# Performance work log

Measured on AMD Instinct MI355X. Metric: run time of the kernel, lower is better.

The kernel has to match this reference:

```python
import jax, jax.numpy as jnp
import numpy as np
import math

HEADS = 10
EPS = 1e-5
SHARED_SCORE_SHIFT = 0.6931471805599453  # log(2)


def expand_first(feat):
    # feat: [B, ...]; batch split into two halves, first element of each half is the style reference
    b = feat.shape[0]
    style = jnp.stack([feat[0], feat[b // 2]])[:, None]  # [2, 1, ...]
    style = jnp.broadcast_to(style, (2, b // 2) + feat.shape[1:])
    return style.reshape(feat.shape)


def adain(feat):
    # feat: [B, H, S, D]; normalize over seq dim (-2), re-style with reference stats
    mean = feat.mean(axis=-2, keepdims=True)
    std = jnp.sqrt(jnp.var(feat, axis=-2, keepdims=True, ddof=1) + EPS)
    style_mean = expand_first(mean)
    style_std = expand_first(std)
    return (feat - mean) / std * style_std + style_mean


def concat_first(feat, axis=2):
    # scale == 1.0 path of concat_first
    return jnp.concatenate([feat, expand_first(feat)], axis=axis)


def setup_inputs() -> dict:
    key = jax.random.key(0)
    ks = jax.random.split(key, 9)
    B, S, C = 4, 1024, 640
    sc = 1.0 / math.sqrt(C)
    return {
        "hidden_states": jax.random.normal(ks[0], (B, S, C), jnp.float32),
        "Wq": jax.random.normal(ks[1], (C, C), jnp.float32) * sc,
        "bq": jax.random.normal(ks[2], (C,), jnp.float32) * 0.01,
        "Wk": jax.random.normal(ks[3], (C, C), jnp.float32) * sc,
        "bk": jax.random.normal(ks[4], (C,), jnp.float32) * 0.01,
        "Wv": jax.random.normal(ks[5], (C, C), jnp.float32) * sc,
        "bv": jax.random.normal(ks[6], (C,), jnp.float32) * 0.01,
        "Wo": jax.random.normal(ks[7], (C, C), jnp.float32) * sc,
        "bo": jax.random.normal(ks[8], (C,), jnp.float32) * 0.01,
    }


def reference(hidden_states, Wq, bq, Wk, bk, Wv, bv, Wo, bo):
    B, S, C = hidden_states.shape
    H = HEADS
    D = C // H
    scale = 1.0 / math.sqrt(D)  # attn.scale

    def split_heads(x):  # [B, S, C] -> [B, H, S, D]
        return x.reshape(B, S, H, D).transpose(0, 2, 1, 3)

    q = split_heads(hidden_states @ Wq.T + bq)
    k = split_heads(hidden_states @ Wk.T + bk)
    v = split_heads(hidden_states @ Wv.T + bv)

    # adain_queries / adain_keys enabled, adain_values disabled
    q = adain(q)
    k = adain(k)

    # shared attention: concatenate reference K/V along seq dim
    k = concat_first(k, axis=2)  # [B, H, 2S, D]
    v = concat_first(v, axis=2)

    logits = jnp.einsum('bhqd,bhkd->bhqk', q, k) * scale
    # additive shift on the shared (appended) keys
    kv_len = k.shape[2]
    shift = jnp.where(jnp.arange(kv_len) >= S, SHARED_SCORE_SHIFT, 0.0).astype(logits.dtype)
    logits = logits + shift
    probs = jax.nn.softmax(logits, axis=-1)
    out = jnp.einsum('bhqk,bhkd->bhqd', probs, v)  # [B, H, S, D]

    out = out.transpose(0, 2, 1, 3).reshape(B, S, C)
    return out @ Wo.T + bo
```

## Files before the change

### kernel.cpp

```cpp
#include <hip/hip_runtime.h>
#include <hip/hip_bf16.h>
#include <math.h>

typedef unsigned short u16;
typedef unsigned int u32;
typedef __attribute__((ext_vector_type(8))) short short8;
typedef __attribute__((ext_vector_type(4))) float float4_;

#define S_LEN 1024
#define C_DIM 640
#define HEADS 10
#define HDIM 64
#define M_TOT 4096
#define WSZ (C_DIM * C_DIM)
#define TX ((size_t)M_TOT * C_DIM)
#define SHIFT_C 0.6931471805599453f
#define LDG 44
#define LDA 76
#define PS  (2 * S_LEN * C_DIM)
#define LS  (2 * HEADS * S_LEN)

static __device__ __forceinline__ float bf2f(u16 u) {
    unsigned int x = ((unsigned int)u) << 16;
    float f; __builtin_memcpy(&f, &x, 4); return f;
}
static __device__ __forceinline__ u16 f2bf(float f) {
    unsigned int x; __builtin_memcpy(&x, &f, 4);
    x = x + 0x7fffu + ((x >> 16) & 1u);
    return (u16)(x >> 16);
}

static __device__ int detect_bf16(const void* X) {
    const u32* p = (const u32*)X;
    int sane = 0;
    for (int i = 0; i < 64; i++) {
        u32 w = p[i];
        int ea = (int)((w >> 7)  & 0xFF);
        int eb = (int)((w >> 23) & 0xFF);
        sane += (ea >= 100 && ea <= 150);
        sane += (eb >= 100 && eb <= 150);
    }
    return sane >= 110;
}

__global__ __launch_bounds__(256) void convert_inputs(
    const void* X, const void* W0, const void* W1, const void* W2, const void* W3,
    const void* B0, const void* B1, const void* B2, const void* B3,
    u16* __restrict__ Xb, u16* __restrict__ Wb, float* __restrict__ Bf,
    int* __restrict__ flag)
{
    __shared__ int is_bf;
    if (threadIdx.x == 0) {
        int f = detect_bf16(X);
        is_bf = f;
        if (blockIdx.x == 0) *flag = f;
    }
    __syncthreads();
    const int f = is_bf;

    const size_t WREG = TX + 4 * (size_t)WSZ;
    const size_t TOT  = WREG + 4 * C_DIM;
    size_t idx8 = ((size_t)blockIdx.x * 256 + threadIdx.x) * 8;
    if (idx8 >= TOT) return;

    const void* src; size_t off; int kind;
    u16* dst16 = nullptr; float* dstf = nullptr;
    if (idx8 < TX) {
        src = X; off = idx8; dst16 = Xb + off; kind = 0;
    } else if (idx8 < WREG) {
        size_t r = idx8 - TX; int w = (int)(r / WSZ); off = r % WSZ;
        src = (w == 0) ? W0 : ((w == 1) ? W1 : ((w == 2) ? W2 : W3));
        dst16 = Wb + (size_t)w * WSZ + off; kind = 0;
    } else {
        size_t r = idx8 - WREG; int w = (int)(r / C_DIM); off = r % C_DIM;
        src = (w == 0) ? B0 : ((w == 1) ? B1 : ((w == 2) ? B2 : B3));
        dstf = Bf + (size_t)w * C_DIM + off; kind = 1;
    }

    if (!f) {
        float4 a = *(const float4*)((const float*)src + off);
        float4 b = *(const float4*)((const float*)src + off + 4);
        if (kind == 0) {
            union { u16 s[8]; uint4 u; } pk;
            pk.s[0] = f2bf(a.x); pk.s[1] = f2bf(a.y); pk.s[2] = f2bf(a.z); pk.s[3] = f2bf(a.w);
            pk.s[4] = f2bf(b.x); pk.s[5] = f2bf(b.y); pk.s[6] = f2bf(b.z); pk.s[7] = f2bf(b.w);
            *(uint4*)dst16 = pk.u;
        } else {
            *(float4*)dstf = a; *(float4*)(dstf + 4) = b;
        }
    } else {
        union { uint4 u; u16 s[8]; } pk;
        pk.u = *(const uint4*)((const u16*)src + off);
        if (kind == 0) {
            *(uint4*)dst16 = pk.u;
        } else {
            #pragma unroll
            for (int j = 0; j < 8; j++) dstf[j] = bf2f(pk.s[j]);
        }
    }
}

__global__ __launch_bounds__(256, 3) void gemm_bt(
    const u16* __restrict__ A, const u16* __restrict__ Wbase,
    const float* __restrict__ Bf,
    u16* Oq, u16* Ok, u16* Vt, float* Of, const int* __restrict__ flag,
    int final_mode)
{
    const int z = final_mode ? 3 : blockIdx.z;
    const u16* W    = Wbase + (size_t)z * WSZ;
    const float* bias = Bf + (size_t)z * C_DIM;

    __shared__ u16 Al[2][128 * LDG];
    __shared__ u16 Wl[2][128 * LDG];

    const int tid  = threadIdx.x;
    const int wave = tid >> 6;
    const int lane = tid & 63;
    const int l16  = lane & 15;
    const int quad = lane >> 4;
    const int m0 = blockIdx.x * 128;
    const int n0 = blockIdx.y * 128;
    const int wm = (wave & 1) * 64;
    const int wn = (wave >> 1) * 64;

    const int srow = tid >> 2;
    const int scol = (tid & 3) * 8;

    float4_ acc[4][4] = {};
    uint4 va[2], vw[2];

    #pragma unroll
    for (int i = 0; i < 2; i++) {
        int row = srow + i * 64;
        va[i] = *(const uint4*)(A + (size_t)(m0 + row) * C_DIM + scol);
        vw[i] = *(const uint4*)(W + (size_t)(n0 + row) * C_DIM + scol);
    }
    #pragma unroll
    for (int i = 0; i < 2; i++) {
        int row = srow + i * 64;
        *(uint4*)(&Al[0][row * LDG + scol]) = va[i];
        *(uint4*)(&Wl[0][row * LDG + scol]) = vw[i];
    }

    const int NIT = C_DIM / 32;
    for (int kt = 0; kt < NIT; kt++) {
        const int buf = kt & 1;
        __syncthreads();

        if (kt + 1 < NIT) {
            int k0 = (kt + 1) * 32;
            #pragma unroll
            for (int i = 0; i < 2; i++) {
                int row = srow + i * 64;
                va[i] = *(const uint4*)(A + (size_t)(m0 + row) * C_DIM + k0 + scol);
                vw[i] = *(const uint4*)(W + (size_t)(n0 + row) * C_DIM + k0 + scol);
            }
        }

        short8 af[4], bfr[4];
        #pragma unroll
        for (int t = 0; t < 4; t++) {
            af[t]  = *(const short8*)(&Al[buf][(wm + t * 16 + l16) * LDG + quad * 8]);
            bfr[t] = *(const short8*)(&Wl[buf][(wn + t * 16 + l16) * LDG + quad * 8]);
        }
        #pragma unroll
        for (int mt = 0; mt < 4; mt++)
            #pragma unroll
            for (int nt = 0; nt < 4; nt++)
                acc[mt][nt] = __builtin_amdgcn_mfma_f32_16x16x32_bf16(
                    af[mt], bfr[nt], acc[mt][nt], 0, 0, 0);

        if (kt + 1 < NIT) {
            #pragma unroll
            for (int i = 0; i < 2; i++) {
                int row = srow + i * 64;
                *(uint4*)(&Al[buf ^ 1][row * LDG + scol]) = va[i];
                *(uint4*)(&Wl[buf ^ 1][row * LDG + scol]) = vw[i];
            }
        }
    }

    const bool wf32 = final_mode && (*flag == 0);
    #pragma unroll
    for (int mt = 0; mt < 4; mt++) {
        #pragma unroll
        for (int nt = 0; nt < 4; nt++) {
            int col = n0 + wn + nt * 16 + l16;
            float bv = bias[col];
            if (!final_mode && z == 2) {
                int row0 = m0 + wm + mt * 16 + quad * 4;
                int bb = row0 >> 10, s = row0 & 1023;
                ushort4 pk;
                pk.x = f2bf(acc[mt][nt][0] + bv);
                pk.y = f2bf(acc[mt][nt][1] + bv);
                pk.z = f2bf(acc[mt][nt][2] + bv);
                pk.w = f2bf(acc[mt][nt][3] + bv);
                *(ushort4*)(Vt + ((size_t)(bb * C_DIM + col)) * S_LEN + s) = pk;
            } else {
                #pragma unroll
                for (int r = 0; r < 4; r++) {
                    int row = m0 + wm + mt * 16 + quad * 4 + r;
                    float val = acc[mt][nt][r] + bv;
                    size_t idx = (size_t)row * C_DIM + col;
                    if (final_mode) {
                        if (wf32) Of[idx] = val;
                        else      Oq[idx] = f2bf(val);
                    } else {
                        u16* Out = (z == 0) ? Oq : Ok;
                        Out[idx] = f2bf(val);
                    }
                }
            }
        }
    }
}

__global__ __launch_bounds__(1024) void adain_stats(
    const u16* __restrict__ Qp, const u16* __restrict__ Kp,
    float* __restrict__ meanArr, float* __restrict__ stdArr)
{
    const int bid = blockIdx.x;
    const int t = bid / 40;
    const int rem = bid % 40;
    const int b = rem / 10;
    const int h = rem % 10;
    const u16* X = t ? Kp : Qp;

    const int tid = threadIdx.x;
    const int do8 = tid & 7;
    const int sg  = tid >> 3;

    const u16* base = X + (size_t)(b * S_LEN) * C_DIM + h * HDIM + do8 * 8;
    float s8[8] = {}, q8[8] = {};
    #pragma unroll
    for (int i = 0; i < 8; i++) {
        int s = sg + i * 128;
        union { uint4 u; u16 e[8]; } v;
        v.u = *(const uint4*)(base + (size_t)s * C_DIM);
        #pragma unroll
        for (int j = 0; j < 8; j++) {
            float f = bf2f(v.e[j]);
            s8[j] += f; q8[j] += f * f;
        }
    }
    #pragma unroll
    for (int off = 8; off < 64; off <<= 1)
        #pragma unroll
        for (int j = 0; j < 8; j++) {
            s8[j] += __shfl_xor(s8[j], off, 64);
            q8[j] += __shfl_xor(q8[j], off, 64);
        }
    __shared__ float ls[16][64], lq[16][64];
    const int wv = tid >> 6, ln = tid & 63;
    if (ln < 8) {
        #pragma unroll
        for (int j = 0; j < 8; j++) { ls[wv][ln * 8 + j] = s8[j]; lq[wv][ln * 8 + j] = q8[j]; }
    }
    __syncthreads();
    if (tid < 64) {
        float Sv = 0.f, Qv = 0.f;
        #pragma unroll
        for (int g = 0; g < 16; g++) { Sv += ls[g][tid]; Qv += lq[g][tid]; }
        float mean = Sv * (1.f / 1024.f);
        float var  = (Qv - Sv * Sv * (1.f / 1024.f)) * (1.f / 1023.f);
        int idx = ((t * 4 + b) * HEADS + h) * HDIM + tid;
        meanArr[idx] = mean;
        stdArr[idx]  = sqrtf(fmaxf(var, 0.f) + 1e-5f);
    }
}

__global__ __launch_bounds__(256) void adain_apply(
    u16* __restrict__ Qp, u16* __restrict__ Kp,
    const float* __restrict__ meanArr, const float* __restrict__ stdArr)
{
    const size_t idx8 = ((size_t)blockIdx.x * 256 + threadIdx.x) * 8;
    const int t  = (int)(idx8 / (2 * S_LEN * C_DIM));
    const int r  = (int)(idx8 % (2 * S_LEN * C_DIM));
    const int bi = r / (S_LEN * C_DIM);
    const int r2 = r % (S_LEN * C_DIM);
    const int s  = r2 / C_DIM;
    const int c  = r2 % C_DIM;
    const int b  = bi * 2 + 1;
    const int h  = c >> 6, d = c & 63;

    u16* X = t ? Kp : Qp;
    const int si   = ((t * 4 + b) * HEADS + h) * HDIM + d;
    const int sref = ((t * 4 + (b - 1)) * HEADS + h) * HDIM + d;

    float4 stT0 = *(const float4*)(stdArr + si);
    float4 stT1 = *(const float4*)(stdArr + si + 4);
    float4 stR0 = *(const float4*)(stdArr + sref);
    float4 stR1 = *(const float4*)(stdArr + sref + 4);
    float4 mnT0 = *(const float4*)(meanArr + si);
    float4 mnT1 = *(const float4*)(meanArr + si + 4);
    float4 mnR0 = *(const float4*)(meanArr + sref);
    float4 mnR1 = *(const float4*)(meanArr + sref + 4);
    float sc[8], of[8];
    sc[0]=stR0.x/stT0.x; sc[1]=stR0.y/stT0.y; sc[2]=stR0.z/stT0.z; sc[3]=stR0.w/stT0.w;
    sc[4]=stR1.x/stT1.x; sc[5]=stR1.y/stT1.y; sc[6]=stR1.z/stT1.z; sc[7]=stR1.w/stT1.w;
    of[0]=mnR0.x-mnT0.x*sc[0]; of[1]=mnR0.y-mnT0.y*sc[1];
    of[2]=mnR0.z-mnT0.z*sc[2]; of[3]=mnR0.w-mnT0.w*sc[3];
    of[4]=mnR1.x-mnT1.x*sc[4]; of[5]=mnR1.y-mnT1.y*sc[5];
    of[6]=mnR1.z-mnT1.z*sc[6]; of[7]=mnR1.w-mnT1.w*sc[7];

    size_t g = (size_t)(b * S_LEN + s) * C_DIM + c;
    union { uint4 u; u16 e[8]; } v;
    v.u = *(const uint4*)(X + g);
    #pragma unroll
    for (int j = 0; j < 8; j++) v.e[j] = f2bf(bf2f(v.e[j]) * sc[j] + of[j]);
    *(uint4*)(X + g) = v.u;
}

__global__ __launch_bounds__(256, 3) void attn_kernel(
    const u16* __restrict__ Q, const u16* __restrict__ K, const u16* __restrict__ VT,
    u16* __restrict__ Oattn, float* __restrict__ Opart, float* __restrict__ lpart)
{
    __shared__ u16 Kl[2][64 * LDA];
    __shared__ u16 Vl[2][64 * LDA];
    __shared__ u16 Pl[4][16 * LDA];

    const int tid  = threadIdx.x;
    const int wave = tid >> 6;
    const int lane = tid & 63;
    const int l16  = lane & 15;
    const int quad = lane >> 4;

    int b, h, qt, p;
    const int bid = blockIdx.x;
    if (bid < 320) {
        p = 0;
        int bh = bid % 40; qt = bid / 40;
        b = bh / HEADS; h = bh % HEADS;
    } else {
        p = 1;
        int rem = bid - 320;
        int t2 = rem % 20; qt = rem / 20;
        b = 1 + 2 * (t2 / HEADS); h = t2 % HEADS;
    }
    const int bs = p ? (b - 1) : b;
    const float shift = p ? SHIFT_C : 0.f;
    const int odd = b & 1;
    const int q0 = qt * 128 + wave * 32;

    short8 qf[2][2];
    #pragma unroll
    for (int qc = 0; qc < 2; qc++) {
        const size_t rowQ = (size_t)(b * S_LEN + q0 + qc * 16 + l16) * C_DIM + h * HDIM;
        qf[qc][0] = *(const short8*)(Q + rowQ + quad * 8);
        qf[qc][1] = *(const short8*)(Q + rowQ + 32 + quad * 8);
    }

    float4_ o[2][4] = {};
    float rs[2] = {0.f, 0.f};

    const int srow = tid >> 3;
    const int sdp  = tid & 7;

    uint4 kreg[2], vreg[2];

    #pragma unroll
    for (int i = 0; i < 2; i++) {
        int row = srow + i * 32;
        kreg[i] = *(const uint4*)(K + (size_t)(bs * S_LEN + row) * C_DIM + h * HDIM + sdp * 8);
        vreg[i] = *(const uint4*)(VT + ((size_t)((bs * HEADS + h) * HDIM) + row) * S_LEN + sdp * 8);
    }
    #pragma unroll
    for (int i = 0; i < 2; i++) {
        int row = srow + i * 32;
        *(uint4*)(&Kl[0][row * LDA + sdp * 8]) = kreg[i];
        *(uint4*)(&Vl[0][row * LDA + sdp * 8]) = vreg[i];
    }

    for (int it = 0; it < 16; it++) {
        const int buf = it & 1;
        __syncthreads();

        if (it + 1 < 16) {
            const int srn = (it + 1) * 64;
            #pragma unroll
            for (int i = 0; i < 2; i++) {
                int row = srow + i * 32;
                kreg[i] = *(const uint4*)(K + (size_t)(bs * S_LEN + srn + row) * C_DIM + h * HDIM + sdp * 8);
                vreg[i] = *(const uint4*)(VT + ((size_t)((bs * HEADS + h) * HDIM) + row) * S_LEN + srn + sdp * 8);
            }
        }

        short8 kf[4][2], vf[2][4];
        #pragma unroll
        for (int nc = 0; nc < 4; nc++) {
            kf[nc][0] = *(const short8*)(&Kl[buf][(nc * 16 + l16) * LDA + quad * 8]);
            kf[nc][1] = *(const short8*)(&Kl[buf][(nc * 16 + l16) * LDA + 32 + quad * 8]);
        }
        #pragma unroll
        for (int kc = 0; kc < 2; kc++)
            #pragma unroll
            for (int dc = 0; dc < 4; dc++)
                vf[kc][dc] = *(const short8*)(&Vl[buf][(dc * 16 + l16) * LDA + kc * 32 + quad * 8]);

        #pragma unroll
        for (int qc = 0; qc < 2; qc++) {
            #pragma unroll
            for (int nc = 0; nc < 4; nc++) {
                float4_ c = {};
                c = __builtin_amdgcn_mfma_f32_16x16x32_bf16(kf[nc][0], qf[qc][0], c, 0, 0, 0);
                c = __builtin_amdgcn_mfma_f32_16x16x32_bf16(kf[nc][1], qf[qc][1], c, 0, 0, 0);
                ushort4 pk;
                #pragma unroll
                for (int r = 0; r < 4; r++) {
                    float pv = __expf(c[r] * 0.125f + shift);
                    rs[qc] += pv;
                    ((u16*)&pk)[r] = f2bf(pv);
                }
                *(ushort4*)(&Pl[wave][l16 * LDA + nc * 16 + quad * 4]) = pk;
            }
            asm volatile("s_waitcnt lgkmcnt(0)" ::: "memory");
            #pragma unroll
            for (int kc = 0; kc < 2; kc++) {
                short8 pf = *(const short8*)(&Pl[wave][l16 * LDA + kc * 32 + quad * 8]);
                #pragma unroll
                for (int dc = 0; dc < 4; dc++)
                    o[qc][dc] = __builtin_amdgcn_mfma_f32_16x16x32_bf16(pf, vf[kc][dc], o[qc][dc], 0, 0, 0);
            }
        }

        if (it + 1 < 16) {
            #pragma unroll
            for (int i = 0; i < 2; i++) {
                int row = srow + i * 32;
                *(uint4*)(&Kl[buf ^ 1][row * LDA + sdp * 8]) = kreg[i];
                *(uint4*)(&Vl[buf ^ 1][row * LDA + sdp * 8]) = vreg[i];
            }
        }
    }

    #pragma unroll
    for (int qc = 0; qc < 2; qc++) {
        rs[qc] += __shfl_xor(rs[qc], 16, 64);
        rs[qc] += __shfl_xor(rs[qc], 32, 64);
    }

    if (odd) {
        const int half = b >> 1;
        float* dst = Opart + (size_t)p * PS;
        #pragma unroll
        for (int qc = 0; qc < 2; qc++) {
            if (quad == 0)
                lpart[(size_t)p * LS + ((size_t)(half * HEADS + h)) * S_LEN + q0 + qc * 16 + l16] = rs[qc];
            #pragma unroll
            for (int dc = 0; dc < 4; dc++)
                #pragma unroll
                for (int r = 0; r < 4; r++) {
                    int qrow = q0 + qc * 16 + quad * 4 + r;
                    dst[((size_t)(half * S_LEN + qrow)) * C_DIM + h * HDIM + dc * 16 + l16] = o[qc][dc][r];
                }
        }
    } else {
        asm volatile("s_waitcnt lgkmcnt(0)" ::: "memory");
        float* Plf = (float*)&Pl[wave][0];
        if (quad == 0) { Plf[l16] = rs[0]; Plf[16 + l16] = rs[1]; }
        asm volatile("s_waitcnt lgkmcnt(0)" ::: "memory");
        #pragma unroll
        for (int qc = 0; qc < 2; qc++) {
            float rl[4];
            #pragma unroll
            for (int r = 0; r < 4; r++) rl[r] = 1.f / Plf[qc * 16 + quad * 4 + r];
            #pragma unroll
            for (int dc = 0; dc < 4; dc++)
                #pragma unroll
                for (int r = 0; r < 4; r++) {
                    size_t row = (size_t)(b * S_LEN + q0 + qc * 16 + quad * 4 + r);
                    Oattn[row * C_DIM + h * HDIM + dc * 16 + l16] = f2bf(o[qc][dc][r] * rl[r]);
                }
        }
    }
}

__global__ __launch_bounds__(256) void attn_merge(
    const float* __restrict__ Opart, const float* __restrict__ lpart,
    u16* __restrict__ Oattn)
{
    const size_t idx8 = ((size_t)blockIdx.x * 256 + threadIdx.x) * 8;
    const int half = (int)(idx8 / (S_LEN * C_DIM));
    const int r2 = (int)(idx8 % (S_LEN * C_DIM));
    const int s = r2 / C_DIM;
    const int c = r2 % C_DIM;
    const int h = c >> 6;

    float l = lpart[((size_t)(half * HEADS + h)) * S_LEN + s]
            + lpart[(size_t)LS + ((size_t)(half * HEADS + h)) * S_LEN + s];
    float rl = 1.f / l;
    float4 a0 = *(const float4*)(Opart + idx8);
    float4 a1 = *(const float4*)(Opart + idx8 + 4);
    float4 b0 = *(const float4*)(Opart + (size_t)PS + idx8);
    float4 b1 = *(const float4*)(Opart + (size_t)PS + idx8 + 4);
    union { u16 e[8]; uint4 u; } pk;
    pk.e[0] = f2bf((a0.x + b0.x) * rl); pk.e[1] = f2bf((a0.y + b0.y) * rl);
    pk.e[2] = f2bf((a0.z + b0.z) * rl); pk.e[3] = f2bf((a0.w + b0.w) * rl);
    pk.e[4] = f2bf((a1.x + b1.x) * rl); pk.e[5] = f2bf((a1.y + b1.y) * rl);
    pk.e[6] = f2bf((a1.z + b1.z) * rl); pk.e[7] = f2bf((a1.w + b1.w) * rl);
    size_t row = (size_t)((1 + 2 * half) * S_LEN + s);
    *(uint4*)(Oattn + row * C_DIM + c) = pk.u;
}

extern "C" void kernel_launch(void* const* d_in, const int* in_sizes, int n_in,
                              void* d_out, int out_size, void* d_ws, size_t ws_size,
                              hipStream_t stream) {
    const void* X  = d_in[0];
    const void* Wq = d_in[1]; const void* bq = d_in[2];
    const void* Wk = d_in[3]; const void* bk = d_in[4];
    const void* Wv = d_in[5]; const void* bv = d_in[6];
    const void* Wo = d_in[7]; const void* bo = d_in[8];

    u16* Xb = (u16*)d_ws;
    u16* q  = Xb + TX;
    u16* k  = q + TX;
    u16* Wb = k + TX;
    float* Bf = (float*)(Wb + 4 * (size_t)WSZ);
    float* meanArr = Bf + 4 * C_DIM;
    float* stdArr  = meanArr + 2 * 4 * HEADS * HDIM;
    int* flagp = (int*)(stdArr + 2 * 4 * HEADS * HDIM);
    float* Opart = (float*)(flagp + 4);
    float* lpart = Opart + 2 * (size_t)PS;
    u16* vt   = (u16*)d_out;
    u16* attn = Xb;

    const size_t TOT = TX + 4 * (size_t)WSZ + 4 * C_DIM;
    convert_inputs<<<(int)((TOT / 8 + 255) / 256), 256, 0, stream>>>(
        X, Wq, Wk, Wv, Wo, bq, bk, bv, bo, Xb, Wb, Bf, flagp);

    dim3 gQKV(M_TOT / 128, C_DIM / 128, 3);
    gemm_bt<<<gQKV, 256, 0, stream>>>(Xb, Wb, Bf, q, k, vt, nullptr, flagp, 0);

    adain_stats<<<80, 1024, 0, stream>>>(q, k, meanArr, stdArr);
    adain_apply<<<(2 * 2 * S_LEN * C_DIM) / (256 * 8), 256, 0, stream>>>(q, k, meanArr, stdArr);

    attn_kernel<<<480, 256, 0, stream>>>(q, k, vt, attn, Opart, lpart);
    attn_merge<<<(2 * S_LEN * C_DIM) / (256 * 8), 256, 0, stream>>>(Opart, lpart, attn);

    dim3 gO(M_TOT / 128, C_DIM / 128, 1);
    gemm_bt<<<gO, 256, 0, stream>>>(attn, Wb, Bf, (u16*)d_out, nullptr, nullptr,
                                    (float*)d_out, flagp, 1);
}
```

Before: 171.0 us.

## Fuse AdaIN apply into attention loads and split-merge into output GEMM

Removes the standalone adain_apply kernel. The per-channel AdaIN affine is now applied to Q fragments and K tiles as they are loaded inside the attention kernel, for odd batches only. Also removes attn_merge: the output projection GEMM now reads the two fp32 partials and their normalizers for odd batches directly in its A-tile loader. This saves two launches and two full read-write passes over memory, at the cost of a branchy A loader that reads 4x more bytes per element in the final GEMM, and repeated affine work per K tile.

```diff
diff --git a/kernel.cpp b/kernel.cpp
--- a/kernel.cpp
+++ b/kernel.cpp
@@ -100,10 +100,37 @@
     }
 }
 
+static __device__ __forceinline__ uint4 ldA(
+    const u16* __restrict__ A, const float* __restrict__ Opart,
+    const float* __restrict__ lpart, int row, int cb, int final_mode)
+{
+    const int batch = row >> 10;
+    if (final_mode && (batch & 1)) {
+        const int half = batch >> 1;
+        const int s = row & 1023;
+        const int h = cb >> 6;
+        size_t li = (size_t)(half * HEADS + h) * S_LEN + s;
+        float rl = 1.f / (lpart[li] + lpart[(size_t)LS + li]);
+        size_t off = ((size_t)(half * S_LEN + s)) * C_DIM + cb;
+        float4 a0 = *(const float4*)(Opart + off);
+        float4 a1 = *(const float4*)(Opart + off + 4);
+        float4 b0 = *(const float4*)(Opart + (size_t)PS + off);
+        float4 b1 = *(const float4*)(Opart + (size_t)PS + off + 4);
+        union { u16 e[8]; uint4 u; } pk;
+        pk.e[0] = f2bf((a0.x + b0.x) * rl); pk.e[1] = f2bf((a0.y + b0.y) * rl);
+        pk.e[2] = f2bf((a0.z + b0.z) * rl); pk.e[3] = f2bf((a0.w + b0.w) * rl);
+        pk.e[4] = f2bf((a1.x + b1.x) * rl); pk.e[5] = f2bf((a1.y + b1.y) * rl);
+        pk.e[6] = f2bf((a1.z + b1.z) * rl); pk.e[7] = f2bf((a1.w + b1.w) * rl);
+        return pk.u;
+    }
+    return *(const uint4*)(A + (size_t)row * C_DIM + cb);
+}
+
 __global__ __launch_bounds__(256, 3) void gemm_bt(
     const u16* __restrict__ A, const u16* __restrict__ Wbase,
     const float* __restrict__ Bf,
     u16* Oq, u16* Ok, u16* Vt, float* Of, const int* __restrict__ flag,
+    const float* __restrict__ Opart, const float* __restrict__ lpart,
     int final_mode)
 {
     const int z = final_mode ? 3 : blockIdx.z;
@@ -132,7 +159,7 @@
     #pragma unroll
     for (int i = 0; i < 2; i++) {
         int row = srow + i * 64;
-        va[i] = *(const uint4*)(A + (size_t)(m0 + row) * C_DIM + scol);
+        va[i] = ldA(A, Opart, lpart, m0 + row, scol, final_mode);
         vw[i] = *(const uint4*)(W + (size_t)(n0 + row) * C_DIM + scol);
     }
     #pragma unroll
@@ -152,7 +179,7 @@
             #pragma unroll
             for (int i = 0; i < 2; i++) {
                 int row = srow + i * 64;
-                va[i] = *(const uint4*)(A + (size_t)(m0 + row) * C_DIM + k0 + scol);
+                va[i] = ldA(A, Opart, lpart, m0 + row, k0 + scol, final_mode);
                 vw[i] = *(const uint4*)(W + (size_t)(n0 + row) * C_DIM + k0 + scol);
             }
         }
@@ -269,50 +296,16 @@
     }
 }
 
-__global__ __launch_bounds__(256) void adain_apply(
-    u16* __restrict__ Qp, u16* __restrict__ Kp,
-    const float* __restrict__ meanArr, const float* __restrict__ stdArr)
-{
-    const size_t idx8 = ((size_t)blockIdx.x * 256 + threadIdx.x) * 8;
-    const int t  = (int)(idx8 / (2 * S_LEN * C_DIM));
-    const int r  = (int)(idx8 % (2 * S_LEN * C_DIM));
-    const int bi = r / (S_LEN * C_DIM);
-    const int r2 = r % (S_LEN * C_DIM);
-    const int s  = r2 / C_DIM;
-    const int c  = r2 % C_DIM;
-    const int b  = bi * 2 + 1;
-    const int h  = c >> 6, d = c & 63;
-
-    u16* X = t ? Kp : Qp;
-    const int si   = ((t * 4 + b) * HEADS + h) * HDIM + d;
-    const int sref = ((t * 4 + (b - 1)) * HEADS + h) * HDIM + d;
-
-    float4 stT0 = *(const float4*)(stdArr + si);
-    float4 stT1 = *(const float4*)(stdArr + si + 4);
-    float4 stR0 = *(const float4*)(stdArr + sref);
-    float4 stR1 = *(const float4*)(stdArr + sref + 4);
-    float4 mnT0 = *(const float4*)(meanArr + si);
-    float4 mnT1 = *(const float4*)(meanArr + si + 4);
-    float4 mnR0 = *(const float4*)(meanArr + sref);
-    float4 mnR1 = *(const float4*)(meanArr + sref + 4);
-    float sc[8], of[8];
-    sc[0]=stR0.x/stT0.x; sc[1]=stR0.y/stT0.y; sc[2]=stR0.z/stT0.z; sc[3]=stR0.w/stT0.w;
-    sc[4]=stR1.x/stT1.x; sc[5]=stR1.y/stT1.y; sc[6]=stR1.z/stT1.z; sc[7]=stR1.w/stT1.w;
-    of[0]=mnR0.x-mnT0.x*sc[0]; of[1]=mnR0.y-mnT0.y*sc[1];
-    of[2]=mnR0.z-mnT0.z*sc[2]; of[3]=mnR0.w-mnT0.w*sc[3];
-    of[4]=mnR1.x-mnT1.x*sc[4]; of[5]=mnR1.y-mnT1.y*sc[5];
-    of[6]=mnR1.z-mnT1.z*sc[6]; of[7]=mnR1.w-mnT1.w*sc[7];
-
-    size_t g = (size_t)(b * S_LEN + s) * C_DIM + c;
-    union { uint4 u; u16 e[8]; } v;
-    v.u = *(const uint4*)(X + g);
-    #pragma unroll
-    for (int j = 0; j < 8; j++) v.e[j] = f2bf(bf2f(v.e[j]) * sc[j] + of[j]);
-    *(uint4*)(X + g) = v.u;
+static __device__ __forceinline__ uint4 affine8(uint4 v, const float* sc, const float* of) {
+    union { uint4 u; u16 e[8]; } x; x.u = v;
+    #pragma unroll
+    for (int j = 0; j < 8; j++) x.e[j] = f2bf(bf2f(x.e[j]) * sc[j] + of[j]);
+    return x.u;
 }
 
 __global__ __launch_bounds__(256, 3) void attn_kernel(
     const u16* __restrict__ Q, const u16* __restrict__ K, const u16* __restrict__ VT,
+    const float* __restrict__ meanArr, const float* __restrict__ stdArr,
     u16* __restrict__ Oattn, float* __restrict__ Opart, float* __restrict__ lpart)
 {
     __shared__ u16 Kl[2][64 * LDA];
@@ -349,12 +342,48 @@
         qf[qc][0] = *(const short8*)(Q + rowQ + quad * 8);
         qf[qc][1] = *(const short8*)(Q + rowQ + 32 + quad * 8);
     }
+    if (odd) {
+        float qsc[2][8], qof[2][8];
+        #pragma unroll
+        for (int ch = 0; ch < 2; ch++) {
+            int dbase = ch * 32 + quad * 8;
+            int si = (b * HEADS + h) * HDIM + dbase;
+            int sr = ((b - 1) * HEADS + h) * HDIM + dbase;
+            #pragma unroll
+            for (int j = 0; j < 8; j++) {
+                float scv = stdArr[sr + j] / stdArr[si + j];
+                qsc[ch][j] = scv;
+                qof[ch][j] = meanArr[sr + j] - meanArr[si + j] * scv;
+            }
+        }
+        #pragma unroll
+        for (int qc = 0; qc < 2; qc++)
+            #pragma unroll
+            for (int ch = 0; ch < 2; ch++) {
+                union { short8 v; uint4 u; } x; x.v = qf[qc][ch];
+                x.u = affine8(x.u, qsc[ch], qof[ch]);
+                qf[qc][ch] = x.v;
+            }
+    }
 
     float4_ o[2][4] = {};
     float rs[2] = {0.f, 0.f};
 
     const int srow = tid >> 3;
     const int sdp  = tid & 7;
+
+    const int kaff = bs & 1;
+    float ksc[8], kof[8];
+    if (kaff) {
+        int si = ((4 + bs) * HEADS + h) * HDIM + sdp * 8;
+        int sr = ((4 + bs - 1) * HEADS + h) * HDIM + sdp * 8;
+        #pragma unroll
+        for (int j = 0; j < 8; j++) {
+            float scv = stdArr[sr + j] / stdArr[si + j];
+            ksc[j] = scv;
+            kof[j] = meanArr[sr + j] - meanArr[si + j] * scv;
+        }
+    }
 
     uint4 kreg[2], vreg[2];
 
@@ -367,7 +396,7 @@
     #pragma unroll
     for (int i = 0; i < 2; i++) {
         int row = srow + i * 32;
-        *(uint4*)(&Kl[0][row * LDA + sdp * 8]) = kreg[i];
+        *(uint4*)(&Kl[0][row * LDA + sdp * 8]) = kaff ? affine8(kreg[i], ksc, kof) : kreg[i];
         *(uint4*)(&Vl[0][row * LDA + sdp * 8]) = vreg[i];
     }
 
@@ -427,7 +456,7 @@
             #pragma unroll
             for (int i = 0; i < 2; i++) {
                 int row = srow + i * 32;
-                *(uint4*)(&Kl[buf ^ 1][row * LDA + sdp * 8]) = kreg[i];
+                *(uint4*)(&Kl[buf ^ 1][row * LDA + sdp * 8]) = kaff ? affine8(kreg[i], ksc, kof) : kreg[i];
                 *(uint4*)(&Vl[buf ^ 1][row * LDA + sdp * 8]) = vreg[i];
             }
         }
@@ -473,33 +502,6 @@
                 }
         }
     }
-}
-
-__global__ __launch_bounds__(256) void attn_merge(
-    const float* __restrict__ Opart, const float* __restrict__ lpart,
-    u16* __restrict__ Oattn)
-{
-    const size_t idx8 = ((size_t)blockIdx.x * 256 + threadIdx.x) * 8;
-    const int half = (int)(idx8 / (S_LEN * C_DIM));
-    const int r2 = (int)(idx8 % (S_LEN * C_DIM));
-    const int s = r2 / C_DIM;
-    const int c = r2 % C_DIM;
-    const int h = c >> 6;
-
-    float l = lpart[((size_t)(half * HEADS + h)) * S_LEN + s]
-            + lpart[(size_t)LS + ((size_t)(half * HEADS + h)) * S_LEN + s];
-    float rl = 1.f / l;
-    float4 a0 = *(const float4*)(Opart + idx8);
-    float4 a1 = *(const float4*)(Opart + idx8 + 4);
-    float4 b0 = *(const float4*)(Opart + (size_t)PS + idx8);
-    float4 b1 = *(const float4*)(Opart + (size_t)PS + idx8 + 4);
-    union { u16 e[8]; uint4 u; } pk;
-    pk.e[0] = f2bf((a0.x + b0.x) * rl); pk.e[1] = f2bf((a0.y + b0.y) * rl);
-    pk.e[2] = f2bf((a0.z + b0.z) * rl); pk.e[3] = f2bf((a0.w + b0.w) * rl);
-    pk.e[4] = f2bf((a1.x + b1.x) * rl); pk.e[5] = f2bf((a1.y + b1.y) * rl);
-    pk.e[6] = f2bf((a1.z + b1.z) * rl); pk.e[7] = f2bf((a1.w + b1.w) * rl);
-    size_t row = (size_t)((1 + 2 * half) * S_LEN + s);
-    *(uint4*)(Oattn + row * C_DIM + c) = pk.u;
 }
 
 extern "C" void kernel_launch(void* const* d_in, const int* in_sizes, int n_in,
@@ -529,15 +531,14 @@
         X, Wq, Wk, Wv, Wo, bq, bk, bv, bo, Xb, Wb, Bf, flagp);
 
     dim3 gQKV(M_TOT / 128, C_DIM / 128, 3);
-    gemm_bt<<<gQKV, 256, 0, stream>>>(Xb, Wb, Bf, q, k, vt, nullptr, flagp, 0);
+    gemm_bt<<<gQKV, 256, 0, stream>>>(Xb, Wb, Bf, q, k, vt, nullptr, flagp,
+                                      nullptr, nullptr, 0);
 
     adain_stats<<<80, 1024, 0, stream>>>(q, k, meanArr, stdArr);
-    adain_apply<<<(2 * 2 * S_LEN * C_DIM) / (256 * 8), 256, 0, stream>>>(q, k, meanArr, stdArr);
-
-    attn_kernel<<<480, 256, 0, stream>>>(q, k, vt, attn, Opart, lpart);
-    attn_merge<<<(2 * S_LEN * C_DIM) / (256 * 8), 256, 0, stream>>>(Opart, lpart, attn);
+
+    attn_kernel<<<480, 256, 0, stream>>>(q, k, vt, meanArr, stdArr, attn, Opart, lpart);
 
     dim3 gO(M_TOT / 128, C_DIM / 128, 1);
     gemm_bt<<<gO, 256, 0, stream>>>(attn, Wb, Bf, (u16*)d_out, nullptr, nullptr,
-                                    (float*)d_out, flagp, 1);
-}
+                                    (float*)d_out, flagp, Opart, lpart, 1);
+}
```

After: 220.3 us. 28.8% more time.
